# Optimization experiments

Hardware: AMD Instinct MI355X
Metric: run time of the kernel (lower is better)

The kernel has to match this reference:

```python
import jax, jax.numpy as jnp
import numpy as np

B, T, L = 32, 512, 16   # clips, transitions per clip, IMU samples per transition
C_IN = 6
H1, H2, H3 = 64, 128, 256
OUT = 256
EPS = 1e-5
SLOPE = 0.1


def setup_inputs() -> dict:
    key = jax.random.key(0)
    ks = jax.random.split(key, 24)
    f32 = jnp.float32

    def n(k, shape, s=0.05):
        return jax.random.normal(k, shape, f32) * s

    inp = {
        "imu": jax.random.normal(ks[0], (B, T, L, C_IN), f32),
        # conv block 1
        "w1": n(ks[1], (H1, C_IN, 3)), "b1": n(ks[2], (H1,)),
        "g1": 1.0 + n(ks[3], (H1,)), "be1": n(ks[4], (H1,)),
        "m1": n(ks[5], (H1,)), "v1": jax.random.uniform(ks[6], (H1,), f32, 0.5, 1.5),
        # conv block 2
        "w2": n(ks[7], (H2, H1, 3)), "b2": n(ks[8], (H2,)),
        "g2": 1.0 + n(ks[9], (H2,)), "be2": n(ks[10], (H2,)),
        "m2": n(ks[11], (H2,)), "v2": jax.random.uniform(ks[12], (H2,), f32, 0.5, 1.5),
        # conv block 3
        "w3": n(ks[13], (H3, H2, 3)), "b3": n(ks[14], (H3,)),
        "g3": 1.0 + n(ks[15], (H3,)), "be3": n(ks[16], (H3,)),
        "m3": n(ks[17], (H3,)), "v3": jax.random.uniform(ks[18], (H3,), f32, 0.5, 1.5),
        # projection (torch Linear: y = x @ W.T + b)
        "wp": n(ks[19], (OUT, H3)), "bp": n(ks[20], (OUT,)),
    }
    return inp


def _conv1d(x, w, b):
    # x: [N, C, L], w: [O, I, K], 'same' padding=1 for K=3
    y = jax.lax.conv_general_dilated(
        x, w, window_strides=(1,), padding=[(1, 1)],
        dimension_numbers=("NCH", "OIH", "NCH"))
    return y + b[None, :, None]


def _block(x, w, b, g, be, m, v):
    # Conv1d -> BatchNorm1d (eval, running stats) -> LeakyReLU(0.1); dropout = identity (eval)
    y = _conv1d(x, w, b)
    y = g[None, :, None] * (y - m[None, :, None]) * jax.lax.rsqrt(v + EPS)[None, :, None] + be[None, :, None]
    return jnp.where(y > 0, y, SLOPE * y)


def reference(imu, w1, b1, g1, be1, m1, v1,
              w2, b2, g2, be2, m2, v2,
              w3, b3, g3, be3, m3, v3,
              wp, bp):
    # Flatten the (batch, transition) double loop into one batched pipeline.
    # imu: [B, T, L, 6] -> [B*T, 6, L]  (= .transpose(0,1).unsqueeze(0) per segment)
    x = imu.reshape(B * T, L, C_IN).transpose(0, 2, 1)
    x = _block(x, w1, b1, g1, be1, m1, v1)
    x = _block(x, w2, b2, g2, be2, m2, v2)
    x = _block(x, w3, b3, g3, be3, m3, v3)   # [B*T, 256, L]
    x = jnp.mean(x, axis=-1)                  # AdaptiveAvgPool1d(1) -> [B*T, 256]
    out = x @ wp.T + bp                       # projection -> [B*T, 256]
    return out.reshape(B, T, OUT)
```

## Files before the change

kernel.cpp:

```cpp
#include <hip/hip_runtime.h>
#include <cstdint>
#include <cstddef>


namespace {

typedef __attribute__((ext_vector_type(8))) short short8;
typedef __attribute__((ext_vector_type(4))) float f32x4;

constexpr int NSEG = 32 * 512;
constexpr float kEps = 1e-5f;

constexpr size_t OFF_A2F = 0;
constexpr size_t OFF_A3F = 49152;
constexpr size_t OFF_WP  = 245760;
constexpr size_t OFF_B2  = 376832;
constexpr size_t OFF_B3  = 377344;
constexpr size_t WS_NEED = 378368;

constexpr int L_ACT2 = 20736;
constexpr int L_POOL = 59904;
constexpr int L_TOTAL = 68352;

__device__ __forceinline__ unsigned short f2bf(float f) {
    union { float f; unsigned int u; } a; a.f = f;
    unsigned int u = a.u + 0x7FFFu + ((a.u >> 16) & 1u);
    return (unsigned short)(u >> 16);
}
__device__ __forceinline__ float bf2f(unsigned short h) {
    union { unsigned int u; float f; } a; a.u = ((unsigned int)h) << 16;
    return a.f;
}

__device__ __forceinline__ void gll16(const void* g, void* l) {
    __builtin_amdgcn_global_load_lds(
        (const __attribute__((address_space(1))) unsigned int*)g,
        (__attribute__((address_space(3))) unsigned int*)l, 16, 0, 0);
}

__device__ __forceinline__ short8 frag16(const void* p) {
    return __builtin_bit_cast(short8, *(const int4*)p);
}

__device__ __forceinline__ void sync_lds() {
    asm volatile("s_waitcnt lgkmcnt(0)" ::: "memory");
    __builtin_amdgcn_s_barrier();
    asm volatile("" ::: "memory");
    __builtin_amdgcn_sched_barrier(0);
}
__device__ __forceinline__ void sync_vm_lds() {
    asm volatile("s_waitcnt vmcnt(0) lgkmcnt(0)" ::: "memory");
    __builtin_amdgcn_s_barrier();
    asm volatile("" ::: "memory");
    __builtin_amdgcn_sched_barrier(0);
}

__device__ __forceinline__ float leaky(float y) { return fmaxf(y, 0.1f * y); }

__global__ __launch_bounds__(256) void k0_prep(
    const float* __restrict__ w2, const float* __restrict__ b2, const float* __restrict__ g2,
    const float* __restrict__ be2, const float* __restrict__ m2, const float* __restrict__ v2,
    const float* __restrict__ w3, const float* __restrict__ b3, const float* __restrict__ g3,
    const float* __restrict__ be3, const float* __restrict__ m3, const float* __restrict__ v3,
    const float* __restrict__ wp, char* __restrict__ ws)
{
    int idx = blockIdx.x * 256 + threadIdx.x;
    if (idx < 3072) {
        int f = idx >> 6, lane = idx & 63;
        int tap = f >> 4, qq = (f >> 3) & 1, rtile = f & 7;
        int row = rtile * 16 + (lane & 15);
        int kb = qq * 32 + (lane >> 4) * 8;
        float a = g2[row] * rsqrtf(v2[row] + kEps);
        unsigned short us[8];
#pragma unroll
        for (int j = 0; j < 8; ++j)
            us[j] = f2bf(a * w2[row * 192 + (kb + j) * 3 + tap]);
        *(int4*)(ws + OFF_A2F + (size_t)idx * 16) = *(const int4*)us;
    } else if (idx < 15360) {
        int u = idx - 3072;
        int f = u >> 6, lane = u & 63;
        int ks = f >> 5, qq = (f >> 4) & 1, rtile = f & 15;
        int tap = ks >> 1, ih = ks & 1;
        int row = rtile * 16 + (lane & 15);
        int kb = qq * 32 + (lane >> 4) * 8;
        float a = g3[row] * rsqrtf(v3[row] + kEps);
        unsigned short us[8];
#pragma unroll
        for (int j = 0; j < 8; ++j) {
            int i = ih * 64 + kb + j;
            us[j] = f2bf(a * w3[row * 384 + i * 3 + tap]);
        }
        *(int4*)(ws + OFF_A3F + (size_t)u * 16) = *(const int4*)us;
    } else if (idx < 23552) {
        int u = idx - 15360;
        int f = u >> 6, lane = u & 63;
        int o = (f >> 3) * 16 + (lane & 15);
        int cb = (f & 7) * 32 + (lane >> 4) * 8;
        unsigned short us[8];
#pragma unroll
        for (int j = 0; j < 8; ++j)
            us[j] = f2bf(wp[o * 256 + cb + j] * 0.0625f);
        *(int4*)(ws + OFF_WP + (size_t)u * 16) = *(const int4*)us;
    } else if (idx < 23680) {
        int o = idx - 23552;
        float a = g2[o] * rsqrtf(v2[o] + kEps);
        ((float*)(ws + OFF_B2))[o] = a * (b2[o] - m2[o]) + be2[o];
    } else if (idx < 23936) {
        int o = idx - 23680;
        float a = g3[o] * rsqrtf(v3[o] + kEps);
        ((float*)(ws + OFF_B3))[o] = a * (b3[o] - m3[o]) + be3[o];
    }
}

__global__ __launch_bounds__(512, 4) void k_all(
    const float* __restrict__ imu,
    const float* __restrict__ w1, const float* __restrict__ b1,
    const float* __restrict__ g1, const float* __restrict__ be1,
    const float* __restrict__ m1, const float* __restrict__ v1,
    const char* __restrict__ ws, const float* __restrict__ bp,
    float* __restrict__ out)
{
    __shared__ char smem[L_TOTAL];
    char* act1L  = smem;
    char* act2L  = smem + L_ACT2;
    char* poolsL = smem + L_POOL;
    char* imuL   = poolsL;
    const char* A2F = ws + OFF_A2F;
    const char* A3F = ws + OFF_A3F;
    const char* WPF = ws + OFF_WP;
    const float* bias2 = (const float*)(ws + OFF_B2);
    const float* bias3 = (const float*)(ws + OFF_B3);

    const int tid = threadIdx.x, lane = tid & 63, wid = tid >> 6;
    const int lo = lane & 15, hi = lane >> 4;
    const int seg0 = blockIdx.x * 8;

    if (wid < 3)
        gll16((const char*)imu + (size_t)seg0 * 384 + wid * 1024 + lane * 16,
              imuL + wid * 1024);
    sync_vm_lds();

    {
        const float* xr = (const float*)imuL + wid * 96;
        const int c = lane;
        const float a = g1[c] * rsqrtf(v1[c] + kEps);
        const float bb = fmaf(a, b1[c] - m1[c], be1[c]);
        float wk[6][3];
#pragma unroll
        for (int i = 0; i < 6; ++i)
#pragma unroll
            for (int k = 0; k < 3; ++k) wk[i][k] = a * w1[c * 18 + i * 3 + k];

        float acc[16];
#pragma unroll
        for (int l = 0; l < 16; ++l) acc[l] = bb;
#pragma unroll
        for (int l = 0; l < 16; ++l) {
            float2 c01 = *(const float2*)(xr + l * 6);
            float2 c23 = *(const float2*)(xr + l * 6 + 2);
            float2 c45 = *(const float2*)(xr + l * 6 + 4);
            float xs6[6] = {c01.x, c01.y, c23.x, c23.y, c45.x, c45.y};
#pragma unroll
            for (int i = 0; i < 6; ++i) {
                float xv = xs6[i];
                if (l > 0)  acc[l - 1] = fmaf(wk[i][2], xv, acc[l - 1]);
                acc[l] = fmaf(wk[i][1], xv, acc[l]);
                if (l < 15) acc[l + 1] = fmaf(wk[i][0], xv, acc[l + 1]);
            }
        }
#pragma unroll
        for (int l = 0; l < 16; ++l)
            *(unsigned short*)(act1L + (wid * 18 + l + 1) * 144 + c * 2) = f2bf(leaky(acc[l]));
        if (tid < 144) {
            int s = tid / 18, rest = tid % 18;
            int h = rest / 9, unit = rest % 9;
            int4 z; z.x = z.y = z.z = z.w = 0;
            *(int4*)(act1L + (s * 18 + h * 17) * 144 + unit * 16) = z;
        }
        if (tid < 272) {
            int s = tid / 34, rest = tid % 34;
            int h = rest / 17, unit = rest % 17;
            int4 z; z.x = z.y = z.z = z.w = 0;
            *(int4*)(act2L + (s * 18 + h * 17) * 272 + unit * 16) = z;
        }
    }

    const int mi2 = wid >> 1, ni2 = wid & 1;
    short8 a2p[2][2];
#pragma unroll
    for (int s = 0; s < 2; ++s)
#pragma unroll
        for (int rt = 0; rt < 2; ++rt)
            a2p[s][rt] = frag16(A2F + (size_t)((s * 8 + mi2 * 2 + rt) * 64 + lane) * 16);

    sync_lds();

    f32x4 acc2[2][4];
#pragma unroll
    for (int i = 0; i < 2; ++i)
#pragma unroll
        for (int j = 0; j < 4; ++j) acc2[i][j] = f32x4{0.f, 0.f, 0.f, 0.f};
    {
        const char* b1base = act1L + lo * 144 + hi * 16;
#pragma unroll
        for (int s = 0; s < 6; ++s) {
            const int tap = s >> 1, qq = s & 1;
            short8 bfr[4];
#pragma unroll
            for (int ct = 0; ct < 4; ++ct)
                bfr[ct] = frag16(b1base + ((ni2 * 4 + ct) * 18 + tap) * 144 + qq * 64);
            __builtin_amdgcn_s_setprio(1);
#pragma unroll
            for (int ct = 0; ct < 4; ++ct) {
                acc2[0][ct] = __builtin_amdgcn_mfma_f32_16x16x32_bf16(a2p[s & 1][0], bfr[ct], acc2[0][ct], 0, 0, 0);
                acc2[1][ct] = __builtin_amdgcn_mfma_f32_16x16x32_bf16(a2p[s & 1][1], bfr[ct], acc2[1][ct], 0, 0, 0);
            }
            __builtin_amdgcn_s_setprio(0);
            if (s < 4) {
#pragma unroll
                for (int rt = 0; rt < 2; ++rt)
                    a2p[s & 1][rt] = frag16(A2F + (size_t)(((s + 2) * 8 + mi2 * 2 + rt) * 64 + lane) * 16);
            }
        }
    }

    const int ni3 = wid >> 1, mi3 = wid & 1;
    short8 w3p[2][4];
#pragma unroll
    for (int s = 0; s < 2; ++s)
#pragma unroll
        for (int ct = 0; ct < 4; ++ct)
            w3p[s][ct] = frag16(A3F + (size_t)((s * 16 + ni3 * 4 + ct) * 64 + lane) * 16);

#pragma unroll
    for (int rt = 0; rt < 2; ++rt) {
        int ch0 = (mi2 * 2 + rt) * 16 + hi * 4;
        float4 b4 = *(const float4*)(bias2 + ch0);
#pragma unroll
        for (int ct = 0; ct < 4; ++ct) {
            float y0 = leaky(acc2[rt][ct][0] + b4.x);
            float y1 = leaky(acc2[rt][ct][1] + b4.y);
            float y2 = leaky(acc2[rt][ct][2] + b4.z);
            float y3 = leaky(acc2[rt][ct][3] + b4.w);
            uint2 pk;
            pk.x = (unsigned int)f2bf(y0) | ((unsigned int)f2bf(y1) << 16);
            pk.y = (unsigned int)f2bf(y2) | ((unsigned int)f2bf(y3) << 16);
            *(uint2*)(act2L + ((ni2 * 4 + ct) * 18 + lo + 1) * 272 + ch0 * 2) = pk;
        }
    }
    sync_lds();

    f32x4 acc3[4][4];
#pragma unroll
    for (int i = 0; i < 4; ++i)
#pragma unroll
        for (int j = 0; j < 4; ++j) acc3[i][j] = f32x4{0.f, 0.f, 0.f, 0.f};
    {
#pragma unroll
        for (int s = 0; s < 12; ++s) {
            const int tap = s >> 2, ih = (s >> 1) & 1, qq = s & 1;
            short8 afr[4];
#pragma unroll
            for (int mt = 0; mt < 4; ++mt)
                afr[mt] = frag16(act2L + ((mi3 * 4 + mt) * 18 + lo + tap) * 272
                                 + ih * 128 + qq * 64 + hi * 16);
            __builtin_amdgcn_s_setprio(1);
#pragma unroll
            for (int mt = 0; mt < 4; ++mt)
#pragma unroll
                for (int ct = 0; ct < 4; ++ct)
                    acc3[mt][ct] = __builtin_amdgcn_mfma_f32_16x16x32_bf16(
                        afr[mt], w3p[s & 1][ct], acc3[mt][ct], 0, 0, 0);
            __builtin_amdgcn_s_setprio(0);
            if (s < 10) {
#pragma unroll
                for (int ct = 0; ct < 4; ++ct)
                    w3p[s & 1][ct] = frag16(A3F + (size_t)(((s + 2) * 16 + ni3 * 4 + ct) * 64 + lane) * 16);
            }
        }
    }

#pragma unroll
    for (int ct = 0; ct < 4; ++ct) {
        int co = (ni3 * 4 + ct) * 16 + lo;
        float bv = bias3[co];
#pragma unroll
        for (int mt = 0; mt < 4; ++mt) {
            float t = 0.f;
#pragma unroll
            for (int r = 0; r < 4; ++r)
                t += leaky(acc3[mt][ct][r] + bv);
            t += __shfl_xor(t, 16, 64);
            t += __shfl_xor(t, 32, 64);
            if (hi == 0) {
                unsigned short ph = f2bf(t);
                unsigned short pl = f2bf(t - bf2f(ph));
                int row = mi3 * 4 + mt;
                *(unsigned short*)(poolsL + row * 528 + co * 2) = ph;
                *(unsigned short*)(poolsL + (row + 8) * 528 + co * 2) = pl;
            }
        }
    }

    short8 wbp[2][2];
#pragma unroll
    for (int q = 0; q < 2; ++q)
#pragma unroll
        for (int ct = 0; ct < 2; ++ct)
            wbp[q][ct] = frag16(WPF + (size_t)(((wid * 2 + ct) * 8 + q) * 64 + lane) * 16);

    sync_lds();

    {
        f32x4 acc4[2];
        acc4[0] = f32x4{0.f, 0.f, 0.f, 0.f};
        acc4[1] = f32x4{0.f, 0.f, 0.f, 0.f};
#pragma unroll
        for (int q = 0; q < 8; ++q) {
            short8 pa = frag16(poolsL + lo * 528 + q * 64 + hi * 16);
            acc4[0] = __builtin_amdgcn_mfma_f32_16x16x32_bf16(pa, wbp[q & 1][0], acc4[0], 0, 0, 0);
            acc4[1] = __builtin_amdgcn_mfma_f32_16x16x32_bf16(pa, wbp[q & 1][1], acc4[1], 0, 0, 0);
            if (q < 6) {
#pragma unroll
                for (int ct = 0; ct < 2; ++ct)
                    wbp[q & 1][ct] = frag16(WPF + (size_t)(((wid * 2 + ct) * 8 + q + 2) * 64 + lane) * 16);
            }
        }
#pragma unroll
        for (int ct = 0; ct < 2; ++ct) {
            int o = (wid * 2 + ct) * 16 + lo;
            float bv = bp[o];
#pragma unroll
            for (int r = 0; r < 4; ++r) {
                float t = acc4[ct][r] + __shfl_xor(acc4[ct][r], 32, 64);
                if (hi < 2)
                    out[(size_t)(seg0 + hi * 4 + r) * 256 + o] = t + bv;
            }
        }
    }
}

}

extern "C" void kernel_launch(void* const* d_in, const int* in_sizes, int n_in,
                              void* d_out, int out_size, void* d_ws, size_t ws_size,
                              hipStream_t stream) {
    if (ws_size < WS_NEED) return;

    const float* imu = (const float*)d_in[0];
    const float* w1 = (const float*)d_in[1];  const float* b1 = (const float*)d_in[2];
    const float* g1 = (const float*)d_in[3];  const float* be1 = (const float*)d_in[4];
    const float* m1 = (const float*)d_in[5];  const float* v1 = (const float*)d_in[6];
    const float* w2 = (const float*)d_in[7];  const float* b2 = (const float*)d_in[8];
    const float* g2 = (const float*)d_in[9];  const float* be2 = (const float*)d_in[10];
    const float* m2 = (const float*)d_in[11]; const float* v2 = (const float*)d_in[12];
    const float* w3 = (const float*)d_in[13]; const float* b3 = (const float*)d_in[14];
    const float* g3 = (const float*)d_in[15]; const float* be3 = (const float*)d_in[16];
    const float* m3 = (const float*)d_in[17]; const float* v3 = (const float*)d_in[18];
    const float* wp = (const float*)d_in[19]; const float* bp = (const float*)d_in[20];
    float* out = (float*)d_out;
    char* ws = (char*)d_ws;

    hipLaunchKernelGGL(k0_prep, dim3(94), dim3(256), 0, stream,
                       w2, b2, g2, be2, m2, v2, w3, b3, g3, be3, m3, v3, wp, ws);
    hipLaunchKernelGGL(k_all, dim3(NSEG / 8), dim3(512), 0, stream,
                       imu, w1, b1, g1, be1, m1, v1, ws, bp, out);
}
```

Measured before the change: 85.86 us.

## Halve block to 4 segments and 4 waves, remapping per-wave MFMA tiles

Each block now handles 4 segments with 256 threads instead of 8 segments with 512, which halves the LDS footprint. The wave-to-tile mappings for conv2, conv3 and the projection are reworked: each wave now covers more output channels over all of the block's segments. Per-wave weight-fragment reuse changes accordingly, and the zero rows of the pooled hi/lo matrix are cleared explicitly. The intent is higher occupancy and more, smaller blocks. Bias and BN parameters are prefetched into registers earlier to hide load latency. The cost is that each block loads weight fragments for only 4 segments, so global/L2 weight traffic per segment doubles, and register pressure rises from the larger per-wave tiles.

Result: slower. 96.99 us (+13.0%).

```diff
diff --git a/kernel.cpp b/kernel.cpp
--- a/kernel.cpp
+++ b/kernel.cpp
@@ -18,9 +18,9 @@
 constexpr size_t OFF_B3  = 377344;
 constexpr size_t WS_NEED = 378368;
 
-constexpr int L_ACT2 = 20736;
-constexpr int L_POOL = 59904;
-constexpr int L_TOTAL = 68352;
+constexpr int L_ACT2 = 10368;
+constexpr int L_POOL = 29952;
+constexpr int L_TOTAL = 38400;
 
 __device__ __forceinline__ unsigned short f2bf(float f) {
     union { float f; unsigned int u; } a; a.f = f;
@@ -112,7 +112,7 @@
     }
 }
 
-__global__ __launch_bounds__(512, 4) void k_all(
+__global__ __launch_bounds__(256, 4) void k_all(
     const float* __restrict__ imu,
     const float* __restrict__ w1, const float* __restrict__ b1,
     const float* __restrict__ g1, const float* __restrict__ be1,
@@ -133,23 +133,28 @@
 
     const int tid = threadIdx.x, lane = tid & 63, wid = tid >> 6;
     const int lo = lane & 15, hi = lane >> 4;
-    const int seg0 = blockIdx.x * 8;
-
-    if (wid < 3)
-        gll16((const char*)imu + (size_t)seg0 * 384 + wid * 1024 + lane * 16,
-              imuL + wid * 1024);
+    const int seg0 = blockIdx.x * 4;
+
+    const int c = lane;
+    float2 w1r[9];
+#pragma unroll
+    for (int t = 0; t < 9; ++t) w1r[t] = *(const float2*)(w1 + c * 18 + t * 2);
+    const float g1v = g1[c], b1v = b1[c], m1v = m1[c], v1v = v1[c], be1v = be1[c];
+
+    if (tid < 96)
+        gll16((const char*)imu + (size_t)seg0 * 384 + tid * 16, imuL + wid * 1024);
     sync_vm_lds();
 
     {
         const float* xr = (const float*)imuL + wid * 96;
-        const int c = lane;
-        const float a = g1[c] * rsqrtf(v1[c] + kEps);
-        const float bb = fmaf(a, b1[c] - m1[c], be1[c]);
+        const float a = g1v * rsqrtf(v1v + kEps);
+        const float bb = fmaf(a, b1v - m1v, be1v);
+        const float* w1f = (const float*)w1r;
         float wk[6][3];
 #pragma unroll
         for (int i = 0; i < 6; ++i)
 #pragma unroll
-            for (int k = 0; k < 3; ++k) wk[i][k] = a * w1[c * 18 + i * 3 + k];
+            for (int k = 0; k < 3; ++k) wk[i][k] = a * w1f[i * 3 + k];
 
         float acc[16];
 #pragma unroll
@@ -171,73 +176,85 @@
 #pragma unroll
         for (int l = 0; l < 16; ++l)
             *(unsigned short*)(act1L + (wid * 18 + l + 1) * 144 + c * 2) = f2bf(leaky(acc[l]));
-        if (tid < 144) {
+        if (tid < 72) {
             int s = tid / 18, rest = tid % 18;
             int h = rest / 9, unit = rest % 9;
             int4 z; z.x = z.y = z.z = z.w = 0;
             *(int4*)(act1L + (s * 18 + h * 17) * 144 + unit * 16) = z;
         }
-        if (tid < 272) {
+        if (tid < 136) {
             int s = tid / 34, rest = tid % 34;
             int h = rest / 17, unit = rest % 17;
             int4 z; z.x = z.y = z.z = z.w = 0;
             *(int4*)(act2L + (s * 18 + h * 17) * 272 + unit * 16) = z;
         }
+        for (int u = tid; u < 264; u += 256) {
+            int row = 8 + u / 33, unit = u % 33;
+            int4 z; z.x = z.y = z.z = z.w = 0;
+            *(int4*)(poolsL + row * 528 + unit * 16) = z;
+        }
     }
 
     const int mi2 = wid >> 1, ni2 = wid & 1;
-    short8 a2p[2][2];
+    short8 a2p[2][4];
 #pragma unroll
     for (int s = 0; s < 2; ++s)
 #pragma unroll
-        for (int rt = 0; rt < 2; ++rt)
-            a2p[s][rt] = frag16(A2F + (size_t)((s * 8 + mi2 * 2 + rt) * 64 + lane) * 16);
+        for (int rt = 0; rt < 4; ++rt)
+            a2p[s][rt] = frag16(A2F + (size_t)((s * 8 + mi2 * 4 + rt) * 64 + lane) * 16);
+    float4 b2r[4];
+#pragma unroll
+    for (int rt = 0; rt < 4; ++rt)
+        b2r[rt] = *(const float4*)(bias2 + (mi2 * 4 + rt) * 16 + hi * 4);
 
     sync_lds();
 
-    f32x4 acc2[2][4];
-#pragma unroll
-    for (int i = 0; i < 2; ++i)
-#pragma unroll
-        for (int j = 0; j < 4; ++j) acc2[i][j] = f32x4{0.f, 0.f, 0.f, 0.f};
+    f32x4 acc2[4][2];
+#pragma unroll
+    for (int i = 0; i < 4; ++i)
+#pragma unroll
+        for (int j = 0; j < 2; ++j) acc2[i][j] = f32x4{0.f, 0.f, 0.f, 0.f};
     {
         const char* b1base = act1L + lo * 144 + hi * 16;
 #pragma unroll
         for (int s = 0; s < 6; ++s) {
             const int tap = s >> 1, qq = s & 1;
-            short8 bfr[4];
-#pragma unroll
-            for (int ct = 0; ct < 4; ++ct)
-                bfr[ct] = frag16(b1base + ((ni2 * 4 + ct) * 18 + tap) * 144 + qq * 64);
+            short8 bfr[2];
+#pragma unroll
+            for (int ct = 0; ct < 2; ++ct)
+                bfr[ct] = frag16(b1base + ((ni2 * 2 + ct) * 18 + tap) * 144 + qq * 64);
             __builtin_amdgcn_s_setprio(1);
 #pragma unroll
-            for (int ct = 0; ct < 4; ++ct) {
-                acc2[0][ct] = __builtin_amdgcn_mfma_f32_16x16x32_bf16(a2p[s & 1][0], bfr[ct], acc2[0][ct], 0, 0, 0);
-                acc2[1][ct] = __builtin_amdgcn_mfma_f32_16x16x32_bf16(a2p[s & 1][1], bfr[ct], acc2[1][ct], 0, 0, 0);
+            for (int rt = 0; rt < 4; ++rt) {
+                acc2[rt][0] = __builtin_amdgcn_mfma_f32_16x16x32_bf16(a2p[s & 1][rt], bfr[0], acc2[rt][0], 0, 0, 0);
+                acc2[rt][1] = __builtin_amdgcn_mfma_f32_16x16x32_bf16(a2p[s & 1][rt], bfr[1], acc2[rt][1], 0, 0, 0);
             }
             __builtin_amdgcn_s_setprio(0);
             if (s < 4) {
 #pragma unroll
-                for (int rt = 0; rt < 2; ++rt)
-                    a2p[s & 1][rt] = frag16(A2F + (size_t)(((s + 2) * 8 + mi2 * 2 + rt) * 64 + lane) * 16);
-            }
-        }
-    }
-
-    const int ni3 = wid >> 1, mi3 = wid & 1;
+                for (int rt = 0; rt < 4; ++rt)
+                    a2p[s & 1][rt] = frag16(A2F + (size_t)(((s + 2) * 8 + mi2 * 4 + rt) * 64 + lane) * 16);
+            }
+        }
+    }
+
     short8 w3p[2][4];
 #pragma unroll
     for (int s = 0; s < 2; ++s)
 #pragma unroll
         for (int ct = 0; ct < 4; ++ct)
-            w3p[s][ct] = frag16(A3F + (size_t)((s * 16 + ni3 * 4 + ct) * 64 + lane) * 16);
-
-#pragma unroll
-    for (int rt = 0; rt < 2; ++rt) {
-        int ch0 = (mi2 * 2 + rt) * 16 + hi * 4;
-        float4 b4 = *(const float4*)(bias2 + ch0);
-#pragma unroll
-        for (int ct = 0; ct < 4; ++ct) {
+            w3p[s][ct] = frag16(A3F + (size_t)((s * 16 + wid * 4 + ct) * 64 + lane) * 16);
+    float b3r[4];
+#pragma unroll
+    for (int ct = 0; ct < 4; ++ct)
+        b3r[ct] = bias3[(wid * 4 + ct) * 16 + lo];
+
+#pragma unroll
+    for (int rt = 0; rt < 4; ++rt) {
+        int ch0 = (mi2 * 4 + rt) * 16 + hi * 4;
+        float4 b4 = b2r[rt];
+#pragma unroll
+        for (int ct = 0; ct < 2; ++ct) {
             float y0 = leaky(acc2[rt][ct][0] + b4.x);
             float y1 = leaky(acc2[rt][ct][1] + b4.y);
             float y2 = leaky(acc2[rt][ct][2] + b4.z);
@@ -245,7 +262,7 @@
             uint2 pk;
             pk.x = (unsigned int)f2bf(y0) | ((unsigned int)f2bf(y1) << 16);
             pk.y = (unsigned int)f2bf(y2) | ((unsigned int)f2bf(y3) << 16);
-            *(uint2*)(act2L + ((ni2 * 4 + ct) * 18 + lo + 1) * 272 + ch0 * 2) = pk;
+            *(uint2*)(act2L + ((ni2 * 2 + ct) * 18 + lo + 1) * 272 + ch0 * 2) = pk;
         }
     }
     sync_lds();
@@ -262,7 +279,7 @@
             short8 afr[4];
 #pragma unroll
             for (int mt = 0; mt < 4; ++mt)
-                afr[mt] = frag16(act2L + ((mi3 * 4 + mt) * 18 + lo + tap) * 272
+                afr[mt] = frag16(act2L + (mt * 18 + lo + tap) * 272
                                  + ih * 128 + qq * 64 + hi * 16);
             __builtin_amdgcn_s_setprio(1);
 #pragma unroll
@@ -275,15 +292,15 @@
             if (s < 10) {
 #pragma unroll
                 for (int ct = 0; ct < 4; ++ct)
-                    w3p[s & 1][ct] = frag16(A3F + (size_t)(((s + 2) * 16 + ni3 * 4 + ct) * 64 + lane) * 16);
+                    w3p[s & 1][ct] = frag16(A3F + (size_t)(((s + 2) * 16 + wid * 4 + ct) * 64 + lane) * 16);
             }
         }
     }
 
 #pragma unroll
     for (int ct = 0; ct < 4; ++ct) {
-        int co = (ni3 * 4 + ct) * 16 + lo;
-        float bv = bias3[co];
+        int co = (wid * 4 + ct) * 16 + lo;
+        float bv = b3r[ct];
 #pragma unroll
         for (int mt = 0; mt < 4; ++mt) {
             float t = 0.f;
@@ -295,46 +312,52 @@
             if (hi == 0) {
                 unsigned short ph = f2bf(t);
                 unsigned short pl = f2bf(t - bf2f(ph));
-                int row = mi3 * 4 + mt;
-                *(unsigned short*)(poolsL + row * 528 + co * 2) = ph;
-                *(unsigned short*)(poolsL + (row + 8) * 528 + co * 2) = pl;
-            }
-        }
-    }
-
-    short8 wbp[2][2];
+                *(unsigned short*)(poolsL + mt * 528 + co * 2) = ph;
+                *(unsigned short*)(poolsL + (mt + 4) * 528 + co * 2) = pl;
+            }
+        }
+    }
+
+    short8 wbp[2][4];
 #pragma unroll
     for (int q = 0; q < 2; ++q)
 #pragma unroll
-        for (int ct = 0; ct < 2; ++ct)
-            wbp[q][ct] = frag16(WPF + (size_t)(((wid * 2 + ct) * 8 + q) * 64 + lane) * 16);
+        for (int ct = 0; ct < 4; ++ct)
+            wbp[q][ct] = frag16(WPF + (size_t)(((wid * 4 + ct) * 8 + q) * 64 + lane) * 16);
+    float bpr[4];
+#pragma unroll
+    for (int ct = 0; ct < 4; ++ct)
+        bpr[ct] = bp[(wid * 4 + ct) * 16 + lo];
 
     sync_lds();
 
     {
-        f32x4 acc4[2];
-        acc4[0] = f32x4{0.f, 0.f, 0.f, 0.f};
-        acc4[1] = f32x4{0.f, 0.f, 0.f, 0.f};
+        f32x4 acc4[4];
+#pragma unroll
+        for (int i = 0; i < 4; ++i) acc4[i] = f32x4{0.f, 0.f, 0.f, 0.f};
 #pragma unroll
         for (int q = 0; q < 8; ++q) {
             short8 pa = frag16(poolsL + lo * 528 + q * 64 + hi * 16);
-            acc4[0] = __builtin_amdgcn_mfma_f32_16x16x32_bf16(pa, wbp[q & 1][0], acc4[0], 0, 0, 0);
-            acc4[1] = __builtin_amdgcn_mfma_f32_16x16x32_bf16(pa, wbp[q & 1][1], acc4[1], 0, 0, 0);
+            __builtin_amdgcn_s_setprio(1);
+#pragma unroll
+            for (int ct = 0; ct < 4; ++ct)
+                acc4[ct] = __builtin_amdgcn_mfma_f32_16x16x32_bf16(pa, wbp[q & 1][ct], acc4[ct], 0, 0, 0);
+            __builtin_amdgcn_s_setprio(0);
             if (q < 6) {
 #pragma unroll
-                for (int ct = 0; ct < 2; ++ct)
-                    wbp[q & 1][ct] = frag16(WPF + (size_t)(((wid * 2 + ct) * 8 + q + 2) * 64 + lane) * 16);
-            }
-        }
-#pragma unroll
-        for (int ct = 0; ct < 2; ++ct) {
-            int o = (wid * 2 + ct) * 16 + lo;
-            float bv = bp[o];
+                for (int ct = 0; ct < 4; ++ct)
+                    wbp[q & 1][ct] = frag16(WPF + (size_t)(((wid * 4 + ct) * 8 + q + 2) * 64 + lane) * 16);
+            }
+        }
+#pragma unroll
+        for (int ct = 0; ct < 4; ++ct) {
+            int o = (wid * 4 + ct) * 16 + lo;
+            float bv = bpr[ct];
 #pragma unroll
             for (int r = 0; r < 4; ++r) {
-                float t = acc4[ct][r] + __shfl_xor(acc4[ct][r], 32, 64);
-                if (hi < 2)
-                    out[(size_t)(seg0 + hi * 4 + r) * 256 + o] = t + bv;
+                float t = acc4[ct][r] + __shfl_xor(acc4[ct][r], 16, 64);
+                if (hi == 0)
+                    out[(size_t)(seg0 + r) * 256 + o] = t + bv;
             }
         }
     }
@@ -363,6 +386,6 @@
 
     hipLaunchKernelGGL(k0_prep, dim3(94), dim3(256), 0, stream,
                        w2, b2, g2, be2, m2, v2, w3, b3, g3, be3, m3, v3, wp, ws);
-    hipLaunchKernelGGL(k_all, dim3(NSEG / 8), dim3(512), 0, stream,
+    hipLaunchKernelGGL(k_all, dim3(NSEG / 4), dim3(256), 0, stream,
                        imu, w1, b1, g1, be1, m1, v1, ws, bp, out);
 }
```

## Compute first conv layer with MFMA via im2col and use packed bf16 conversion

Applied to the files above, without the earlier changes.

Replaces the scalar FMA implementation of conv block 1 with an im2col staging buffer in LDS and bf16 MFMA instructions. The layer-1 weights are folded with BatchNorm and pre-packed in the prep kernel. Software bf16 rounding is replaced by the hardware v_cvt_pk_bf16_f32 instruction in all epilogues, and the bias3 loads are hoisted. The change adds an extra barrier and about 10KB more LDS per block, which could reduce occupancy. It also quantizes the layer-1 inputs and weights to bf16.

Measured after the change: 82.03 us. 4.5% less time.

```diff
diff --git a/kernel.cpp b/kernel.cpp
--- a/kernel.cpp
+++ b/kernel.cpp
@@ -16,20 +16,28 @@
 constexpr size_t OFF_WP  = 245760;
 constexpr size_t OFF_B2  = 376832;
 constexpr size_t OFF_B3  = 377344;
-constexpr size_t WS_NEED = 378368;
+constexpr size_t OFF_A1F = 378368;
+constexpr size_t OFF_B1C = 382464;
+constexpr size_t WS_NEED = 382720;
 
 constexpr int L_ACT2 = 20736;
-constexpr int L_POOL = 59904;
-constexpr int L_TOTAL = 68352;
+constexpr int L_IMC  = 59904;
+constexpr int L_POOL = 70144;
+constexpr int L_TOTAL = 78592;
 
 __device__ __forceinline__ unsigned short f2bf(float f) {
     union { float f; unsigned int u; } a; a.f = f;
     unsigned int u = a.u + 0x7FFFu + ((a.u >> 16) & 1u);
     return (unsigned short)(u >> 16);
 }
-__device__ __forceinline__ float bf2f(unsigned short h) {
-    union { unsigned int u; float f; } a; a.u = ((unsigned int)h) << 16;
-    return a.f;
+
+__device__ __forceinline__ unsigned int cvt_pk_bf16(float a, float b) {
+    unsigned int r;
+    asm("v_cvt_pk_bf16_f32 %0, %1, %2" : "=v"(r) : "v"(a), "v"(b));
+    return r;
+}
+__device__ __forceinline__ float asf(unsigned int u) {
+    union { unsigned int u; float f; } a; a.u = u; return a.f;
 }
 
 __device__ __forceinline__ void gll16(const void* g, void* l) {
@@ -58,6 +66,8 @@
 __device__ __forceinline__ float leaky(float y) { return fmaxf(y, 0.1f * y); }
 
 __global__ __launch_bounds__(256) void k0_prep(
+    const float* __restrict__ w1, const float* __restrict__ b1, const float* __restrict__ g1,
+    const float* __restrict__ be1, const float* __restrict__ m1, const float* __restrict__ v1,
     const float* __restrict__ w2, const float* __restrict__ b2, const float* __restrict__ g2,
     const float* __restrict__ be2, const float* __restrict__ m2, const float* __restrict__ v2,
     const float* __restrict__ w3, const float* __restrict__ b3, const float* __restrict__ g3,
@@ -109,20 +119,34 @@
         int o = idx - 23680;
         float a = g3[o] * rsqrtf(v3[o] + kEps);
         ((float*)(ws + OFF_B3))[o] = a * (b3[o] - m3[o]) + be3[o];
+    } else if (idx < 24192) {
+        int u = idx - 23936;
+        int f = u >> 6, lane = u & 63;
+        int row = f * 16 + (lane & 15);
+        float a = g1[row] * rsqrtf(v1[row] + kEps);
+        unsigned short us[8];
+#pragma unroll
+        for (int j = 0; j < 8; ++j) {
+            int k = (lane >> 4) * 8 + j;
+            us[j] = (k < 18) ? f2bf(a * w1[row * 18 + k]) : (unsigned short)0;
+        }
+        *(int4*)(ws + OFF_A1F + (size_t)u * 16) = *(const int4*)us;
+    } else if (idx < 24256) {
+        int o = idx - 24192;
+        float a = g1[o] * rsqrtf(v1[o] + kEps);
+        ((float*)(ws + OFF_B1C))[o] = a * (b1[o] - m1[o]) + be1[o];
     }
 }
 
 __global__ __launch_bounds__(512, 4) void k_all(
     const float* __restrict__ imu,
-    const float* __restrict__ w1, const float* __restrict__ b1,
-    const float* __restrict__ g1, const float* __restrict__ be1,
-    const float* __restrict__ m1, const float* __restrict__ v1,
     const char* __restrict__ ws, const float* __restrict__ bp,
     float* __restrict__ out)
 {
     __shared__ char smem[L_TOTAL];
     char* act1L  = smem;
     char* act2L  = smem + L_ACT2;
+    char* imcL   = smem + L_IMC;
     char* poolsL = smem + L_POOL;
     char* imuL   = poolsL;
     const char* A2F = ws + OFF_A2F;
@@ -135,42 +159,59 @@
     const int lo = lane & 15, hi = lane >> 4;
     const int seg0 = blockIdx.x * 8;
 
+    short8 a1p[4];
+#pragma unroll
+    for (int m = 0; m < 4; ++m)
+        a1p[m] = frag16(ws + OFF_A1F + (size_t)(m * 64 + lane) * 16);
+    float4 bb4[4];
+#pragma unroll
+    for (int m = 0; m < 4; ++m)
+        bb4[m] = *(const float4*)((const float*)(ws + OFF_B1C) + m * 16 + hi * 4);
+
     if (wid < 3)
         gll16((const char*)imu + (size_t)seg0 * 384 + wid * 1024 + lane * 16,
               imuL + wid * 1024);
     sync_vm_lds();
 
     {
-        const float* xr = (const float*)imuL + wid * 96;
-        const int c = lane;
-        const float a = g1[c] * rsqrtf(v1[c] + kEps);
-        const float bb = fmaf(a, b1[c] - m1[c], be1[c]);
-        float wk[6][3];
-#pragma unroll
-        for (int i = 0; i < 6; ++i)
-#pragma unroll
-            for (int k = 0; k < 3; ++k) wk[i][k] = a * w1[c * 18 + i * 3 + k];
-
-        float acc[16];
-#pragma unroll
-        for (int l = 0; l < 16; ++l) acc[l] = bb;
-#pragma unroll
-        for (int l = 0; l < 16; ++l) {
-            float2 c01 = *(const float2*)(xr + l * 6);
-            float2 c23 = *(const float2*)(xr + l * 6 + 2);
-            float2 c45 = *(const float2*)(xr + l * 6 + 4);
-            float xs6[6] = {c01.x, c01.y, c23.x, c23.y, c45.x, c45.y};
-#pragma unroll
-            for (int i = 0; i < 6; ++i) {
-                float xv = xs6[i];
-                if (l > 0)  acc[l - 1] = fmaf(wk[i][2], xv, acc[l - 1]);
-                acc[l] = fmaf(wk[i][1], xv, acc[l]);
-                if (l < 15) acc[l + 1] = fmaf(wk[i][0], xv, acc[l + 1]);
-            }
-        }
-#pragma unroll
-        for (int l = 0; l < 16; ++l)
-            *(unsigned short*)(act1L + (wid * 18 + l + 1) * 144 + c * 2) = f2bf(leaky(acc[l]));
+        const float* xf = (const float*)imuL;
+        const int kq = wid & 3;
+        const int col = (wid >> 2) * 64 + lane;
+        const int seg = col >> 4, l = col & 15;
+        const float* xb = xf + seg * 96 + l * 6;
+        float v[8];
+        if (kq == 0) {
+            v[0] = l > 0  ? xb[-6] : 0.f;
+            v[1] = xb[0];
+            v[2] = l < 15 ? xb[6]  : 0.f;
+            v[3] = l > 0  ? xb[-5] : 0.f;
+            v[4] = xb[1];
+            v[5] = l < 15 ? xb[7]  : 0.f;
+            v[6] = l > 0  ? xb[-4] : 0.f;
+            v[7] = xb[2];
+        } else if (kq == 1) {
+            v[0] = l < 15 ? xb[8]  : 0.f;
+            v[1] = l > 0  ? xb[-3] : 0.f;
+            v[2] = xb[3];
+            v[3] = l < 15 ? xb[9]  : 0.f;
+            v[4] = l > 0  ? xb[-2] : 0.f;
+            v[5] = xb[4];
+            v[6] = l < 15 ? xb[10] : 0.f;
+            v[7] = l > 0  ? xb[-1] : 0.f;
+        } else if (kq == 2) {
+            v[0] = xb[5];
+            v[1] = l < 15 ? xb[11] : 0.f;
+            v[2] = v[3] = v[4] = v[5] = v[6] = v[7] = 0.f;
+        } else {
+            v[0] = v[1] = v[2] = v[3] = v[4] = v[5] = v[6] = v[7] = 0.f;
+        }
+        uint4 pk;
+        pk.x = cvt_pk_bf16(v[0], v[1]);
+        pk.y = cvt_pk_bf16(v[2], v[3]);
+        pk.z = cvt_pk_bf16(v[4], v[5]);
+        pk.w = cvt_pk_bf16(v[6], v[7]);
+        *(uint4*)(imcL + seg * 1280 + l * 80 + kq * 16) = pk;
+
         if (tid < 144) {
             int s = tid / 18, rest = tid % 18;
             int h = rest / 9, unit = rest % 9;
@@ -182,6 +223,30 @@
             int h = rest / 17, unit = rest % 17;
             int4 z; z.x = z.y = z.z = z.w = 0;
             *(int4*)(act2L + (s * 18 + h * 17) * 272 + unit * 16) = z;
+        }
+    }
+    sync_lds();
+
+    {
+        f32x4 acc1[4];
+#pragma unroll
+        for (int m = 0; m < 4; ++m) acc1[m] = f32x4{0.f, 0.f, 0.f, 0.f};
+        short8 bq = frag16(imcL + wid * 1280 + lo * 80 + hi * 16);
+        __builtin_amdgcn_s_setprio(1);
+#pragma unroll
+        for (int m = 0; m < 4; ++m)
+            acc1[m] = __builtin_amdgcn_mfma_f32_16x16x32_bf16(a1p[m], bq, acc1[m], 0, 0, 0);
+        __builtin_amdgcn_s_setprio(0);
+#pragma unroll
+        for (int m = 0; m < 4; ++m) {
+            float y0 = leaky(acc1[m][0] + bb4[m].x);
+            float y1 = leaky(acc1[m][1] + bb4[m].y);
+            float y2 = leaky(acc1[m][2] + bb4[m].z);
+            float y3 = leaky(acc1[m][3] + bb4[m].w);
+            uint2 pk;
+            pk.x = cvt_pk_bf16(y0, y1);
+            pk.y = cvt_pk_bf16(y2, y3);
+            *(uint2*)(act1L + (wid * 18 + lo + 1) * 144 + m * 32 + hi * 8) = pk;
         }
     }
 
@@ -231,6 +296,10 @@
 #pragma unroll
         for (int ct = 0; ct < 4; ++ct)
             w3p[s][ct] = frag16(A3F + (size_t)((s * 16 + ni3 * 4 + ct) * 64 + lane) * 16);
+    float b3r[4];
+#pragma unroll
+    for (int ct = 0; ct < 4; ++ct)
+        b3r[ct] = bias3[(ni3 * 4 + ct) * 16 + lo];
 
 #pragma unroll
     for (int rt = 0; rt < 2; ++rt) {
@@ -243,8 +312,8 @@
             float y2 = leaky(acc2[rt][ct][2] + b4.z);
             float y3 = leaky(acc2[rt][ct][3] + b4.w);
             uint2 pk;
-            pk.x = (unsigned int)f2bf(y0) | ((unsigned int)f2bf(y1) << 16);
-            pk.y = (unsigned int)f2bf(y2) | ((unsigned int)f2bf(y3) << 16);
+            pk.x = cvt_pk_bf16(y0, y1);
+            pk.y = cvt_pk_bf16(y2, y3);
             *(uint2*)(act2L + ((ni2 * 4 + ct) * 18 + lo + 1) * 272 + ch0 * 2) = pk;
         }
     }
@@ -283,22 +352,37 @@
 #pragma unroll
     for (int ct = 0; ct < 4; ++ct) {
         int co = (ni3 * 4 + ct) * 16 + lo;
-        float bv = bias3[co];
+        float bv = b3r[ct];
+        float t[4];
 #pragma unroll
         for (int mt = 0; mt < 4; ++mt) {
-            float t = 0.f;
+            float s4 = 0.f;
 #pragma unroll
             for (int r = 0; r < 4; ++r)
-                t += leaky(acc3[mt][ct][r] + bv);
-            t += __shfl_xor(t, 16, 64);
-            t += __shfl_xor(t, 32, 64);
-            if (hi == 0) {
-                unsigned short ph = f2bf(t);
-                unsigned short pl = f2bf(t - bf2f(ph));
-                int row = mi3 * 4 + mt;
-                *(unsigned short*)(poolsL + row * 528 + co * 2) = ph;
-                *(unsigned short*)(poolsL + (row + 8) * 528 + co * 2) = pl;
-            }
+                s4 += leaky(acc3[mt][ct][r] + bv);
+            s4 += __shfl_xor(s4, 16, 64);
+            s4 += __shfl_xor(s4, 32, 64);
+            t[mt] = s4;
+        }
+        unsigned int pkA = cvt_pk_bf16(t[0], t[1]);
+        unsigned int pkB = cvt_pk_bf16(t[2], t[3]);
+        float r0 = t[0] - asf(pkA << 16);
+        float r1 = t[1] - asf(pkA & 0xffff0000u);
+        float r2 = t[2] - asf(pkB << 16);
+        float r3 = t[3] - asf(pkB & 0xffff0000u);
+        unsigned int pkrA = cvt_pk_bf16(r0, r1);
+        unsigned int pkrB = cvt_pk_bf16(r2, r3);
+        if (hi == 0) {
+            int row0 = mi3 * 4;
+            char* pc = poolsL + co * 2;
+            *(unsigned short*)(pc + (row0 + 0) * 528) = (unsigned short)pkA;
+            *(unsigned short*)(pc + (row0 + 1) * 528) = (unsigned short)(pkA >> 16);
+            *(unsigned short*)(pc + (row0 + 2) * 528) = (unsigned short)pkB;
+            *(unsigned short*)(pc + (row0 + 3) * 528) = (unsigned short)(pkB >> 16);
+            *(unsigned short*)(pc + (row0 + 8) * 528) = (unsigned short)pkrA;
+            *(unsigned short*)(pc + (row0 + 9) * 528) = (unsigned short)(pkrA >> 16);
+            *(unsigned short*)(pc + (row0 + 10) * 528) = (unsigned short)pkrB;
+            *(unsigned short*)(pc + (row0 + 11) * 528) = (unsigned short)(pkrB >> 16);
         }
     }
 
@@ -361,8 +445,9 @@
     float* out = (float*)d_out;
     char* ws = (char*)d_ws;
 
-    hipLaunchKernelGGL(k0_prep, dim3(94), dim3(256), 0, stream,
+    hipLaunchKernelGGL(k0_prep, dim3(95), dim3(256), 0, stream,
+                       w1, b1, g1, be1, m1, v1,
                        w2, b2, g2, be2, m2, v2, w3, b3, g3, be3, m3, v3, wp, ws);
     hipLaunchKernelGGL(k_all, dim3(NSEG / 8), dim3(512), 0, stream,
-                       imu, w1, b1, g1, be1, m1, v1, ws, bp, out);
-}
+                       imu, ws, bp, out);
+}
```
